# Performance work log

Measured on AMD Instinct MI355X. Metric: run time of the kernel, lower is better.

## Reference

```python
import jax, jax.numpy as jnp
import numpy as np

IN_DIM = 512
HID = 512
OUT_DIM = 512
NUM_LEVELS = 8
N_NODES = 32768
LN_EPS = 1e-5


def setup_inputs() -> dict:
    key = jax.random.key(0)
    ks = jax.random.split(key, 12)
    s_in = 1.0 / np.sqrt(IN_DIM)
    s_h = 1.0 / np.sqrt(HID)
    s_2h = 1.0 / np.sqrt(2 * HID)
    return {
        "node_features": jax.random.normal(ks[0], (N_NODES, IN_DIM), dtype=jnp.float32),
        "node_levels": jax.random.randint(ks[1], (N_NODES,), 0, NUM_LEVELS),
        # per-level projections (torch Linear stored transposed: [in, out])
        "W_proj": jax.random.uniform(ks[2], (NUM_LEVELS, IN_DIM, HID), minval=-s_in, maxval=s_in),
        "b_proj": jax.random.uniform(ks[3], (NUM_LEVELS, HID), minval=-s_in, maxval=s_in),
        # inter-level attention MLP: Linear(2h->h) split into current/level halves
        "W1a": jax.random.uniform(ks[4], (HID, HID), minval=-s_2h, maxval=s_2h),
        "W1b": jax.random.uniform(ks[5], (HID, HID), minval=-s_2h, maxval=s_2h),
        "b1": jax.random.uniform(ks[6], (HID,), minval=-s_2h, maxval=s_2h),
        "w2": jax.random.uniform(ks[7], (HID,), minval=-s_h, maxval=s_h),
        "b2": jax.random.uniform(ks[8], (), minval=-s_h, maxval=s_h),
        # output projection + LayerNorm
        "Wout": jax.random.uniform(ks[9], (HID, OUT_DIM), minval=-s_h, maxval=s_h),
        "bout": jax.random.uniform(ks[10], (OUT_DIM,), minval=-s_h, maxval=s_h),
        "gamma": jnp.ones((OUT_DIM,), dtype=jnp.float32),
        "beta": jnp.zeros((OUT_DIM,), dtype=jnp.float32),
    }


def reference(node_features, node_levels, W_proj, b_proj, W1a, W1b, b1, w2, b2,
              Wout, bout, gamma, beta):
    L = W_proj.shape[0]
    N = node_features.shape[0]
    onehot = jax.nn.one_hot(node_levels, L, dtype=node_features.dtype)  # [N, L]

    # Per-level projections, selected by each node's level (vectorizes the first loop).
    h = jnp.zeros((N, W_proj.shape[2]), dtype=node_features.dtype)
    for lvl in range(L):  # small fixed loop over structurally distinct weights
        h = h + onehot[:, lvl:lvl + 1] * (node_features @ W_proj[lvl] + b_proj[lvl])

    # Level means (computed once instead of per-node).
    counts = jnp.sum(onehot, axis=0)                      # [L]
    means = (onehot.T @ h) / jnp.maximum(counts, 1.0)[:, None]  # [L, HID]

    # Attention: score(i, l) = w2 . tanh(h_i @ W1a + mean_l @ W1b + b1) + b2
    A = h @ W1a          # [N, HID]
    B = means @ W1b      # [L, HID]
    pre = jnp.tanh(A[:, None, :] + B[None, :, :] + b1)    # [N, L, HID]
    scores = jnp.einsum('nlh,h->nl', pre, w2) + b2        # [N, L]
    scores = jnp.where(counts[None, :] > 0, scores, -jnp.inf)  # empty levels skipped
    wts = jax.nn.softmax(scores, axis=1)                  # [N, L]
    enhanced = wts @ means                                # [N, HID]

    # Output projection + LayerNorm + ReLU (dropout is identity at eval).
    o = enhanced @ Wout + bout
    mu = jnp.mean(o, axis=-1, keepdims=True)
    var = jnp.mean(jnp.square(o - mu), axis=-1, keepdims=True)
    o = (o - mu) * jax.lax.rsqrt(var + LN_EPS) * gamma + beta
    return jax.nn.relu(o)
```

## Files before the change

### kernel.cpp

```cpp
#include <hip/hip_runtime.h>
#include <hip/hip_bf16.h>
#include <math.h>

#define NN 32768
#define D 512
#define NL 8
#define BM 128
#define PADMAX 33792
#define MT_MAX 264

typedef __attribute__((ext_vector_type(8))) short short8;
typedef __attribute__((ext_vector_type(8))) __bf16 bf16x8;
typedef __attribute__((ext_vector_type(4))) float f32x4;
typedef __attribute__((ext_vector_type(4))) unsigned short us4;

__device__ __forceinline__ unsigned short f2bf(float f){
  unsigned u = __builtin_bit_cast(unsigned, f);
  u += 0x7FFFu + ((u>>16)&1u);
  return (unsigned short)(u>>16);
}
__device__ __forceinline__ float bf2f(unsigned short s){
  return __builtin_bit_cast(float, ((unsigned)s)<<16);
}
__device__ __forceinline__ float tanh_fast(float x){
  float e = __expf(2.f*x);
  return 1.f - 2.f*__builtin_amdgcn_rcpf(1.f+e);
}

__global__ void k_zero(float* w0){
  int t = blockIdx.x*blockDim.x + threadIdx.x;
  for(int i=t;i<4160;i+=gridDim.x*blockDim.x) w0[i]=0.f;
}

__global__ void k_hist(const int* __restrict__ lv, int* __restrict__ counts){
  __shared__ int h[NL];
  if(threadIdx.x<NL) h[threadIdx.x]=0;
  __syncthreads();
  for(int i=blockIdx.x*blockDim.x+threadIdx.x; i<NN; i+=gridDim.x*blockDim.x)
    atomicAdd(&h[lv[i]],1);
  __syncthreads();
  if(threadIdx.x<NL) atomicAdd(&counts[threadIdx.x], h[threadIdx.x]);
}

__global__ void k_offsets(const int* __restrict__ counts, int* __restrict__ poff, int* __restrict__ cursors){
  if(threadIdx.x==0 && blockIdx.x==0){
    int acc=0;
    for(int l=0;l<NL;l++){ poff[l]=acc; cursors[l]=acc; acc += (counts[l]+BM-1)/BM*BM; }
    poff[NL]=acc;
  }
}

__global__ __launch_bounds__(256) void k_scatter(const int* __restrict__ lv, int* __restrict__ cursors, int* __restrict__ perm){
  __shared__ int h[NL];
  __shared__ int base[NL];
  int t = threadIdx.x;
  if(t<NL) h[t]=0;
  __syncthreads();
  int i = blockIdx.x*256 + t;
  int lvl = 0, rank = 0;
  if(i<NN){ lvl = lv[i]; rank = atomicAdd(&h[lvl],1); }
  __syncthreads();
  if(t<NL) base[t] = (h[t]>0) ? atomicAdd(&cursors[t], h[t]) : 0;
  __syncthreads();
  if(i<NN) perm[base[lvl] + rank] = i;
}

__global__ __launch_bounds__(256) void k_trans(const float* __restrict__ Wp, const float* __restrict__ W1a,
                                               unsigned short* __restrict__ WtP, unsigned short* __restrict__ Wt1a){
  int m = blockIdx.z;
  const float* src = (m<NL)? Wp + (size_t)m*D*D : W1a;
  unsigned short* dst = (m<NL)? WtP + (size_t)m*D*D : Wt1a;
  __shared__ unsigned short t[64][68];
  int k0=blockIdx.x*64, n0=blockIdx.y*64;
  int c = threadIdx.x&63, r4 = threadIdx.x>>6;
  for(int p=0;p<64;p+=4){ int r=p+r4; t[r][c] = f2bf(src[(size_t)(k0+r)*D + n0+c]); }
  __syncthreads();
  for(int p=0;p<64;p+=4){ int r=p+r4; dst[(size_t)(n0+r)*D + k0+c] = t[c][r]; }
}

__global__ __launch_bounds__(128) void k_gather(const float* __restrict__ X, const int* __restrict__ perm,
                                                const int* __restrict__ poff, const int* __restrict__ counts,
                                                unsigned short* __restrict__ Xg){
  int r = blockIdx.x, t = threadIdx.x;
  int total = poff[NL];
  int idx = -1;
  if(r<total){
    int lvl=0; while(r>=poff[lvl+1]) lvl++;
    if(r - poff[lvl] < counts[lvl]) idx = perm[r];
  }
  us4 pv = (us4){0,0,0,0};
  if(idx>=0){
    f32x4 x = *(const f32x4*)(X + (size_t)idx*D + t*4);
    #pragma unroll
    for(int e=0;e<4;e++) pv[e] = f2bf(x[e]);
  }
  *(us4*)(Xg + (size_t)r*D + t*4) = pv;
}

template<bool PROJ>
__global__ __launch_bounds__(256) void k_gemm(
    const unsigned short* __restrict__ Xs,
    const unsigned short* __restrict__ Wt,
    const float* __restrict__ bias,
    unsigned short* __restrict__ Out,
    float* __restrict__ sums,
    const int* __restrict__ poff,
    const int* __restrict__ counts)
{
  __shared__ unsigned short Asb[BM*64];
  __shared__ unsigned short Bsb[64*64];
  __shared__ float lsum[64];
  int row0 = blockIdx.x*BM;
  int total = poff[NL];
  if(row0 >= total) return;
  int n0 = blockIdx.y*64;
  int lvl = 0;
  if(PROJ){ while(row0 >= poff[lvl+1]) lvl++; }
  const unsigned short* Wb = PROJ ? (Wt + (size_t)lvl*D*D) : Wt;
  int tid = threadIdx.x;
  if(PROJ && tid<64) lsum[tid]=0.f;
  int l = tid&63, w=tid>>6;
  int wm = w>>1, wn = w&1;
  int l15 = l&15, lhi = l>>4;
  f32x4 acc[4][2];
  #pragma unroll
  for(int i=0;i<4;i++)
    #pragma unroll
    for(int j=0;j<2;j++) acc[i][j] = (f32x4){0.f,0.f,0.f,0.f};

  for(int kt=0;kt<D/64;kt++){
    int k0 = kt*64;
    #pragma unroll
    for(int p=0;p<4;p++){
      int flat = p*256+tid;
      int ar = flat>>3, ag = flat&7;
      short8 v = *(const short8*)(Xs + (size_t)(row0+ar)*D + k0 + ag*8);
      *(short8*)(Asb + ar*64 + ((ag^(ar&7))<<3)) = v;
    }
    #pragma unroll
    for(int p=0;p<2;p++){
      int flat = p*256+tid;
      int br = flat>>3, bg = flat&7;
      short8 v = *(const short8*)(Wb + (size_t)(n0+br)*D + k0 + bg*8);
      *(short8*)(Bsb + br*64 + ((bg^(br&7))<<3)) = v;
    }
    __syncthreads();
    #pragma unroll
    for(int kk=0;kk<2;kk++){
      int swz = ((kk*4+lhi) ^ (l15&7))<<3;
      bf16x8 a[4], b[2];
      #pragma unroll
      for(int fm=0;fm<4;fm++)
        a[fm] = __builtin_bit_cast(bf16x8, *(const short8*)(Asb + (wm*64+fm*16+l15)*64 + swz));
      #pragma unroll
      for(int fn=0;fn<2;fn++)
        b[fn] = __builtin_bit_cast(bf16x8, *(const short8*)(Bsb + (wn*32+fn*16+l15)*64 + swz));
      #pragma unroll
      for(int fm=0;fm<4;fm++)
        #pragma unroll
        for(int fn=0;fn<2;fn++)
          acc[fm][fn] = __builtin_amdgcn_mfma_f32_16x16x32_bf16(a[fm], b[fn], acc[fm][fn], 0,0,0);
    }
    __syncthreads();
  }
  int cnt=0, pb=0;
  if(PROJ){ cnt = counts[lvl]; pb = poff[lvl]; }
  float csum[2] = {0.f,0.f};
  #pragma unroll
  for(int fn=0;fn<2;fn++){
    int col = n0 + wn*32 + fn*16 + l15;
    float bia = PROJ ? bias[lvl*D + col] : 0.f;
    #pragma unroll
    for(int fm=0;fm<4;fm++){
      #pragma unroll
      for(int j=0;j<4;j++){
        int grow = row0 + wm*64 + fm*16 + lhi*4 + j;
        float v = acc[fm][fn][j] + bia;
        Out[(size_t)grow*D + col] = f2bf(v);
        if(PROJ && (grow-pb)<cnt) csum[fn] += v;
      }
    }
  }
  if(PROJ){
    #pragma unroll
    for(int fn=0;fn<2;fn++){
      float s = csum[fn];
      s += __shfl_xor(s,16);
      s += __shfl_xor(s,32);
      if(lhi==0) atomicAdd(&lsum[wn*32+fn*16+l15], s);
    }
    __syncthreads();
    if(tid<64) atomicAdd(&sums[(size_t)lvl*D + n0 + tid], lsum[tid]);
  }
}

__global__ __launch_bounds__(128) void k_small(
    const float* __restrict__ sums, const int* __restrict__ counts,
    const float* __restrict__ W1b, const float* __restrict__ b1,
    const float* __restrict__ Wout, float* __restrict__ Bpre, float* __restrict__ MW)
{
  int lvl = blockIdx.x, jc = blockIdx.y, t = threadIdx.x;
  __shared__ float mean[D];
  int c = counts[lvl];
  float inv = 1.f / (float)(c>0?c:1);
  for(int k=t;k<D;k+=128) mean[k] = sums[lvl*D+k]*inv;
  __syncthreads();
  int j = jc*128 + t;
  float a=0.f, b=0.f;
  for(int k=0;k<D;k++){ float m = mean[k]; a += m*W1b[(size_t)k*D+j]; b += m*Wout[(size_t)k*D+j]; }
  Bpre[lvl*D+j] = a + b1[j];
  MW[lvl*D+j] = b;
}

__global__ __launch_bounds__(256) void k_score(
    const unsigned short* __restrict__ Ag, const int* __restrict__ perm,
    const int* __restrict__ poff, const int* __restrict__ counts,
    const float* __restrict__ Bpre, const float* __restrict__ MW,
    const float* __restrict__ w2, const float* __restrict__ b2,
    const float* __restrict__ bout, const float* __restrict__ gamma,
    const float* __restrict__ beta, float* __restrict__ out)
{
  int l = threadIdx.x & 63;
  int r = blockIdx.x*4 + (threadIdx.x>>6);
  int total = poff[NL];
  if(r >= total) return;
  int lvl=0; while(r>=poff[lvl+1]) lvl++;
  if(r - poff[lvl] >= counts[lvl]) return;
  int orig = perm[r];
  short8 av = *(const short8*)(Ag + (size_t)r*D + l*8);
  float a[8], w2v[8];
  #pragma unroll
  for(int e=0;e<8;e++){ a[e] = bf2f((unsigned short)av[e]); w2v[e] = w2[l*8+e]; }
  float sc[NL];
  #pragma unroll
  for(int lev=0;lev<NL;lev++){
    float s = 0.f;
    #pragma unroll
    for(int e=0;e<8;e++) s += w2v[e]*tanh_fast(a[e] + Bpre[lev*D + l*8 + e]);
    #pragma unroll
    for(int off=1; off<64; off<<=1) s += __shfl_xor(s, off);
    sc[lev] = s;
  }
  float b2v = b2[0];
  float mx = -1e30f;
  #pragma unroll
  for(int lev=0;lev<NL;lev++){ sc[lev]+=b2v; if(counts[lev]>0) mx = fmaxf(mx, sc[lev]); }
  float den=0.f, wts[NL];
  #pragma unroll
  for(int lev=0;lev<NL;lev++){ float e = (counts[lev]>0) ? __expf(sc[lev]-mx) : 0.f; wts[lev]=e; den+=e; }
  float iden = 1.f/den;
  #pragma unroll
  for(int lev=0;lev<NL;lev++) wts[lev]*=iden;
  float o[8]; float s1=0.f;
  #pragma unroll
  for(int q=0;q<8;q++){
    int c = l + 64*q;
    float v = bout[c];
    #pragma unroll
    for(int lev=0;lev<NL;lev++) v += wts[lev]*MW[lev*D + c];
    o[q]=v; s1+=v;
  }
  #pragma unroll
  for(int off=1; off<64; off<<=1) s1 += __shfl_xor(s1,off);
  float mu = s1 * (1.f/512.f);
  float s2=0.f;
  #pragma unroll
  for(int q=0;q<8;q++){ float d=o[q]-mu; s2 += d*d; }
  #pragma unroll
  for(int off=1; off<64; off<<=1) s2 += __shfl_xor(s2,off);
  float rs = rsqrtf(s2*(1.f/512.f) + 1e-5f);
  #pragma unroll
  for(int q=0;q<8;q++){
    int c = l + 64*q;
    float y = (o[q]-mu)*rs*gamma[c] + beta[c];
    out[(size_t)orig*D + c] = fmaxf(y, 0.f);
  }
}

extern "C" void kernel_launch(void* const* d_in, const int* in_sizes, int n_in,
                              void* d_out, int out_size, void* d_ws, size_t ws_size,
                              hipStream_t stream) {
  (void)in_sizes; (void)n_in; (void)out_size; (void)ws_size;
  const float* X    = (const float*)d_in[0];
  const int*   lv   = (const int*)  d_in[1];
  const float* Wp   = (const float*)d_in[2];
  const float* bp   = (const float*)d_in[3];
  const float* W1a  = (const float*)d_in[4];
  const float* W1b  = (const float*)d_in[5];
  const float* b1   = (const float*)d_in[6];
  const float* w2   = (const float*)d_in[7];
  const float* b2   = (const float*)d_in[8];
  const float* Wout = (const float*)d_in[9];
  const float* bout = (const float*)d_in[10];
  const float* gmma = (const float*)d_in[11];
  const float* beta = (const float*)d_in[12];
  float* out = (float*)d_out;

  char* ws = (char*)d_ws;
  int*   counts  = (int*)(ws+0);
  int*   cursors = (int*)(ws+64);
  int*   poff    = (int*)(ws+128);
  float* sums    = (float*)(ws+256);
  float* Bpre    = (float*)(ws+16640);
  float* MW      = (float*)(ws+33024);
  int*   perm    = (int*)(ws+49664);
  unsigned short* WtP  = (unsigned short*)(ws+186368);
  unsigned short* Wt1a = WtP + (size_t)NL*D*D;
  unsigned short* Xg   = (unsigned short*)(ws+4905472);
  unsigned short* Hg   = (unsigned short*)(ws+39508480);
  unsigned short* Ag   = Xg;

  k_zero   <<<dim3(9),   dim3(512), 0, stream>>>((float*)ws);
  k_hist   <<<dim3(64),  dim3(256), 0, stream>>>(lv, counts);
  k_offsets<<<dim3(1),   dim3(64),  0, stream>>>(counts, poff, cursors);
  k_scatter<<<dim3(128), dim3(256), 0, stream>>>(lv, cursors, perm);
  k_trans  <<<dim3(8,8,9), dim3(256), 0, stream>>>(Wp, W1a, WtP, Wt1a);
  k_gather <<<dim3(PADMAX), dim3(128), 0, stream>>>(X, perm, poff, counts, Xg);
  k_gemm<true> <<<dim3(MT_MAX,8), dim3(256), 0, stream>>>(Xg, WtP, bp, Hg, sums, poff, counts);
  k_small  <<<dim3(8,4), dim3(128), 0, stream>>>(sums, counts, W1b, b1, Wout, Bpre, MW);
  k_gemm<false><<<dim3(MT_MAX,8), dim3(256), 0, stream>>>(Hg, Wt1a, nullptr, Ag, sums, poff, counts);
  k_score  <<<dim3(PADMAX/4), dim3(256), 0, stream>>>(Ag, perm, poff, counts, Bpre, MW,
                                                      w2, b2, bout, gmma, beta, out);
}
```

Measured before the change: 323.0 us.

## Widen GEMM tile to 128 columns with direct global-to-LDS loads; batch score rows

The GEMM kernel now uses a 128x128 output tile, with each wave computing a 4x4 grid of MFMA fragments. Tiles are staged through global_load_lds straight into LDS, so the register round-trip and the XOR swizzle are gone. The score kernel now handles four rows per wave, loading Bpre and MW once and reusing them across those rows with vectorized loads. The aim is to cut global traffic and instruction overhead. In exchange, the unswizzled LDS layout may cause bank conflicts, accumulator register pressure rises, and the grid has fewer blocks.

```diff
diff --git a/kernel.cpp b/kernel.cpp
--- a/kernel.cpp
+++ b/kernel.cpp
@@ -6,6 +6,7 @@
 #define D 512
 #define NL 8
 #define BM 128
+#define BN 128
 #define PADMAX 33792
 #define MT_MAX 264
 
@@ -13,6 +14,10 @@
 typedef __attribute__((ext_vector_type(8))) __bf16 bf16x8;
 typedef __attribute__((ext_vector_type(4))) float f32x4;
 typedef __attribute__((ext_vector_type(4))) unsigned short us4;
+
+#define GLDS16(gsrc, ldst) __builtin_amdgcn_global_load_lds( \
+    (const __attribute__((address_space(1))) unsigned int*)(gsrc), \
+    (__attribute__((address_space(3))) unsigned int*)(ldst), 16, 0, 0)
 
 __device__ __forceinline__ unsigned short f2bf(float f){
   unsigned u = __builtin_bit_cast(unsigned, f);
@@ -107,68 +112,61 @@
     const int* __restrict__ poff,
     const int* __restrict__ counts)
 {
-  __shared__ unsigned short Asb[BM*64];
-  __shared__ unsigned short Bsb[64*64];
-  __shared__ float lsum[64];
+  __shared__ __attribute__((aligned(16))) unsigned short Asb[BM*64];
+  __shared__ __attribute__((aligned(16))) unsigned short Bsb[BN*64];
+  __shared__ float lsum[BN];
   int row0 = blockIdx.x*BM;
-  int total = poff[NL];
-  if(row0 >= total) return;
-  int n0 = blockIdx.y*64;
+  if(row0 >= poff[NL]) return;
+  int n0 = blockIdx.y*BN;
   int lvl = 0;
   if(PROJ){ while(row0 >= poff[lvl+1]) lvl++; }
   const unsigned short* Wb = PROJ ? (Wt + (size_t)lvl*D*D) : Wt;
   int tid = threadIdx.x;
-  if(PROJ && tid<64) lsum[tid]=0.f;
-  int l = tid&63, w=tid>>6;
+  if(PROJ && tid<BN) lsum[tid]=0.f;
+  int l = tid&63, w = tid>>6;
   int wm = w>>1, wn = w&1;
   int l15 = l&15, lhi = l>>4;
-  f32x4 acc[4][2];
+  int lo = (l>>3)*D + (l&7)*8;
+  const unsigned short* Abase = Xs + (size_t)row0*D + lo;
+  const unsigned short* Bbase = Wb + (size_t)n0*D + lo;
+  f32x4 acc[4][4];
   #pragma unroll
   for(int i=0;i<4;i++)
     #pragma unroll
-    for(int j=0;j<2;j++) acc[i][j] = (f32x4){0.f,0.f,0.f,0.f};
+    for(int j=0;j<4;j++) acc[i][j] = (f32x4){0.f,0.f,0.f,0.f};
 
   for(int kt=0;kt<D/64;kt++){
     int k0 = kt*64;
     #pragma unroll
-    for(int p=0;p<4;p++){
-      int flat = p*256+tid;
-      int ar = flat>>3, ag = flat&7;
-      short8 v = *(const short8*)(Xs + (size_t)(row0+ar)*D + k0 + ag*8);
-      *(short8*)(Asb + ar*64 + ((ag^(ar&7))<<3)) = v;
-    }
-    #pragma unroll
-    for(int p=0;p<2;p++){
-      int flat = p*256+tid;
-      int br = flat>>3, bg = flat&7;
-      short8 v = *(const short8*)(Wb + (size_t)(n0+br)*D + k0 + bg*8);
-      *(short8*)(Bsb + br*64 + ((bg^(br&7))<<3)) = v;
-    }
+    for(int i=0;i<4;i++)
+      GLDS16(Abase + (size_t)((w*4+i)*8)*D + k0, Asb + (w*4+i)*512);
+    #pragma unroll
+    for(int i=0;i<4;i++)
+      GLDS16(Bbase + (size_t)((w*4+i)*8)*D + k0, Bsb + (w*4+i)*512);
     __syncthreads();
     #pragma unroll
     for(int kk=0;kk<2;kk++){
-      int swz = ((kk*4+lhi) ^ (l15&7))<<3;
-      bf16x8 a[4], b[2];
+      bf16x8 af[4], bg[4];
       #pragma unroll
       for(int fm=0;fm<4;fm++)
-        a[fm] = __builtin_bit_cast(bf16x8, *(const short8*)(Asb + (wm*64+fm*16+l15)*64 + swz));
-      #pragma unroll
-      for(int fn=0;fn<2;fn++)
-        b[fn] = __builtin_bit_cast(bf16x8, *(const short8*)(Bsb + (wn*32+fn*16+l15)*64 + swz));
+        af[fm] = __builtin_bit_cast(bf16x8, *(const short8*)(Asb + (wm*64+fm*16+l15)*64 + kk*32 + lhi*8));
+      #pragma unroll
+      for(int fn=0;fn<4;fn++)
+        bg[fn] = __builtin_bit_cast(bf16x8, *(const short8*)(Bsb + (wn*64+fn*16+l15)*64 + kk*32 + lhi*8));
       #pragma unroll
       for(int fm=0;fm<4;fm++)
         #pragma unroll
-        for(int fn=0;fn<2;fn++)
-          acc[fm][fn] = __builtin_amdgcn_mfma_f32_16x16x32_bf16(a[fm], b[fn], acc[fm][fn], 0,0,0);
+        for(int fn=0;fn<4;fn++)
+          acc[fm][fn] = __builtin_amdgcn_mfma_f32_16x16x32_bf16(af[fm], bg[fn], acc[fm][fn], 0,0,0);
     }
     __syncthreads();
   }
   int cnt=0, pb=0;
   if(PROJ){ cnt = counts[lvl]; pb = poff[lvl]; }
-  float csum[2] = {0.f,0.f};
-  #pragma unroll
-  for(int fn=0;fn<2;fn++){
-    int col = n0 + wn*32 + fn*16 + l15;
+  float csum[4] = {0.f,0.f,0.f,0.f};
+  #pragma unroll
+  for(int fn=0;fn<4;fn++){
+    int col = n0 + wn*64 + fn*16 + l15;
     float bia = PROJ ? bias[lvl*D + col] : 0.f;
     #pragma unroll
     for(int fm=0;fm<4;fm++){
@@ -183,14 +181,14 @@
   }
   if(PROJ){
     #pragma unroll
-    for(int fn=0;fn<2;fn++){
+    for(int fn=0;fn<4;fn++){
       float s = csum[fn];
       s += __shfl_xor(s,16);
       s += __shfl_xor(s,32);
-      if(lhi==0) atomicAdd(&lsum[wn*32+fn*16+l15], s);
+      if(lhi==0) atomicAdd(&lsum[wn*64+fn*16+l15], s);
     }
     __syncthreads();
-    if(tid<64) atomicAdd(&sums[(size_t)lvl*D + n0 + tid], lsum[tid]);
+    if(tid<BN) atomicAdd(&sums[(size_t)lvl*D + n0 + tid], lsum[tid]);
   }
 }
 
@@ -221,59 +219,103 @@
     const float* __restrict__ beta, float* __restrict__ out)
 {
   int l = threadIdx.x & 63;
-  int r = blockIdx.x*4 + (threadIdx.x>>6);
+  int r0 = blockIdx.x*16 + (threadIdx.x>>6)*4;
   int total = poff[NL];
-  if(r >= total) return;
-  int lvl=0; while(r>=poff[lvl+1]) lvl++;
-  if(r - poff[lvl] >= counts[lvl]) return;
-  int orig = perm[r];
-  short8 av = *(const short8*)(Ag + (size_t)r*D + l*8);
-  float a[8], w2v[8];
-  #pragma unroll
-  for(int e=0;e<8;e++){ a[e] = bf2f((unsigned short)av[e]); w2v[e] = w2[l*8+e]; }
-  float sc[NL];
+  if(r0 >= total) return;
+  int lvl=0; while(r0>=poff[lvl+1]) lvl++;
+  int pb = poff[lvl], cnt = counts[lvl];
+  if(r0 - pb >= cnt) return;
+  int val[4], orig[4];
+  #pragma unroll
+  for(int r=0;r<4;r++){
+    val[r] = (r0+r-pb) < cnt;
+    orig[r] = val[r] ? perm[r0+r] : 0;
+  }
+  f32x4 w2a = *(const f32x4*)(w2 + l*8);
+  f32x4 w2b = *(const f32x4*)(w2 + l*8 + 4);
+  float a[4][8];
+  #pragma unroll
+  for(int r=0;r<4;r++){
+    short8 av = *(const short8*)(Ag + (size_t)(r0+r)*D + l*8);
+    #pragma unroll
+    for(int e=0;e<8;e++) a[r][e] = bf2f((unsigned short)av[e]);
+  }
+  int cl[NL];
+  #pragma unroll
+  for(int lev=0;lev<NL;lev++) cl[lev]=counts[lev];
+  float sc[4][NL];
   #pragma unroll
   for(int lev=0;lev<NL;lev++){
-    float s = 0.f;
-    #pragma unroll
-    for(int e=0;e<8;e++) s += w2v[e]*tanh_fast(a[e] + Bpre[lev*D + l*8 + e]);
-    #pragma unroll
-    for(int off=1; off<64; off<<=1) s += __shfl_xor(s, off);
-    sc[lev] = s;
-  }
+    f32x4 b0 = *(const f32x4*)(Bpre + lev*D + l*8);
+    f32x4 b1v = *(const f32x4*)(Bpre + lev*D + l*8 + 4);
+    #pragma unroll
+    for(int r=0;r<4;r++){
+      float s = 0.f;
+      #pragma unroll
+      for(int e=0;e<4;e++) s += w2a[e]*tanh_fast(a[r][e]+b0[e]);
+      #pragma unroll
+      for(int e=0;e<4;e++) s += w2b[e]*tanh_fast(a[r][4+e]+b1v[e]);
+      sc[r][lev] = s;
+    }
+  }
+  #pragma unroll
+  for(int r=0;r<4;r++)
+    #pragma unroll
+    for(int lev=0;lev<NL;lev++){
+      float s = sc[r][lev];
+      #pragma unroll
+      for(int off=1;off<64;off<<=1) s += __shfl_xor(s,off);
+      sc[r][lev] = s;
+    }
   float b2v = b2[0];
-  float mx = -1e30f;
-  #pragma unroll
-  for(int lev=0;lev<NL;lev++){ sc[lev]+=b2v; if(counts[lev]>0) mx = fmaxf(mx, sc[lev]); }
-  float den=0.f, wts[NL];
-  #pragma unroll
-  for(int lev=0;lev<NL;lev++){ float e = (counts[lev]>0) ? __expf(sc[lev]-mx) : 0.f; wts[lev]=e; den+=e; }
-  float iden = 1.f/den;
-  #pragma unroll
-  for(int lev=0;lev<NL;lev++) wts[lev]*=iden;
-  float o[8]; float s1=0.f;
+  #pragma unroll
+  for(int r=0;r<4;r++){
+    float mx=-1e30f;
+    #pragma unroll
+    for(int lev=0;lev<NL;lev++){ sc[r][lev]+=b2v; if(cl[lev]>0) mx=fmaxf(mx,sc[r][lev]); }
+    float den=0.f;
+    #pragma unroll
+    for(int lev=0;lev<NL;lev++){ float e=(cl[lev]>0)?__expf(sc[r][lev]-mx):0.f; sc[r][lev]=e; den+=e; }
+    float id=1.f/den;
+    #pragma unroll
+    for(int lev=0;lev<NL;lev++) sc[r][lev]*=id;
+  }
+  float o[4][8];
   #pragma unroll
   for(int q=0;q<8;q++){
     int c = l + 64*q;
-    float v = bout[c];
-    #pragma unroll
-    for(int lev=0;lev<NL;lev++) v += wts[lev]*MW[lev*D + c];
-    o[q]=v; s1+=v;
-  }
-  #pragma unroll
-  for(int off=1; off<64; off<<=1) s1 += __shfl_xor(s1,off);
-  float mu = s1 * (1.f/512.f);
-  float s2=0.f;
-  #pragma unroll
-  for(int q=0;q<8;q++){ float d=o[q]-mu; s2 += d*d; }
-  #pragma unroll
-  for(int off=1; off<64; off<<=1) s2 += __shfl_xor(s2,off);
-  float rs = rsqrtf(s2*(1.f/512.f) + 1e-5f);
-  #pragma unroll
-  for(int q=0;q<8;q++){
-    int c = l + 64*q;
-    float y = (o[q]-mu)*rs*gamma[c] + beta[c];
-    out[(size_t)orig*D + c] = fmaxf(y, 0.f);
+    float bo = bout[c];
+    #pragma unroll
+    for(int r=0;r<4;r++) o[r][q]=bo;
+    #pragma unroll
+    for(int lev=0;lev<NL;lev++){
+      float m = MW[lev*D+c];
+      #pragma unroll
+      for(int r=0;r<4;r++) o[r][q] += sc[r][lev]*m;
+    }
+  }
+  #pragma unroll
+  for(int r=0;r<4;r++){
+    if(!val[r]) continue;
+    float s1=0.f;
+    #pragma unroll
+    for(int q=0;q<8;q++) s1+=o[r][q];
+    #pragma unroll
+    for(int off=1;off<64;off<<=1) s1 += __shfl_xor(s1,off);
+    float mu = s1*(1.f/512.f);
+    float s2=0.f;
+    #pragma unroll
+    for(int q=0;q<8;q++){ float d=o[r][q]-mu; s2+=d*d; }
+    #pragma unroll
+    for(int off=1;off<64;off<<=1) s2 += __shfl_xor(s2,off);
+    float rs = rsqrtf(s2*(1.f/512.f)+1e-5f);
+    size_t ob = (size_t)orig[r]*D;
+    #pragma unroll
+    for(int q=0;q<8;q++){
+      int c = l+64*q;
+      float y = (o[r][q]-mu)*rs*gamma[c]+beta[c];
+      out[ob+c] = fmaxf(y,0.f);
+    }
   }
 }
 
@@ -316,9 +358,9 @@
   k_scatter<<<dim3(128), dim3(256), 0, stream>>>(lv, cursors, perm);
   k_trans  <<<dim3(8,8,9), dim3(256), 0, stream>>>(Wp, W1a, WtP, Wt1a);
   k_gather <<<dim3(PADMAX), dim3(128), 0, stream>>>(X, perm, poff, counts, Xg);
-  k_gemm<true> <<<dim3(MT_MAX,8), dim3(256), 0, stream>>>(Xg, WtP, bp, Hg, sums, poff, counts);
+  k_gemm<true> <<<dim3(MT_MAX,4), dim3(256), 0, stream>>>(Xg, WtP, bp, Hg, sums, poff, counts);
   k_small  <<<dim3(8,4), dim3(128), 0, stream>>>(sums, counts, W1b, b1, Wout, Bpre, MW);
-  k_gemm<false><<<dim3(MT_MAX,8), dim3(256), 0, stream>>>(Hg, Wt1a, nullptr, Ag, sums, poff, counts);
-  k_score  <<<dim3(PADMAX/4), dim3(256), 0, stream>>>(Ag, perm, poff, counts, Bpre, MW,
-                                                      w2, b2, bout, gmma, beta, out);
-}
+  k_gemm<false><<<dim3(MT_MAX,4), dim3(256), 0, stream>>>(Hg, Wt1a, nullptr, Ag, sums, poff, counts);
+  k_score  <<<dim3(PADMAX/16), dim3(256), 0, stream>>>(Ag, perm, poff, counts, Bpre, MW,
+                                                       w2, b2, bout, gmma, beta, out);
+}
```

Result: slower. 334.9 us (+3.7%).
